# Performance work log

Measured on AMD Instinct MI355X. Metric: run time of the kernel, lower is better.

## Reference

```python
import jax, jax.numpy as jnp
import numpy as np

# Counts-based indexed grouped linear (canonical 'uv,u,v' path of
# SegmentedPolynomialIndexedLinear): tokens x[z] are sorted by group idx[z];
# output y[z] = coeff * x[z] @ W[idx[z]] where W = w.reshape(C, U, V).

C, U, V, Z = 8, 512, 512, 32768


def setup_inputs() -> dict:
    key = jax.random.key(0)
    kw, kx, ki = jax.random.split(key, 3)
    w = jax.random.normal(kw, (C, U * V), dtype=jnp.float32)  # [C, u*v] per-group weights
    x = jax.random.normal(kx, (Z, U), dtype=jnp.float32)      # [Z, u] tokens
    idx = jnp.sort(jax.random.randint(ki, (Z,), 0, C))        # sorted group ids (module asserts sortedness)
    coefficients = jnp.ones((1,), dtype=jnp.float32)          # path coefficient buffer
    return {"w": w, "x": x, "idx": idx, "coefficients": coefficients}


def reference(w, x, idx, coefficients):
    C_ = w.shape[0]
    Zt, U_ = x.shape
    V_ = w.shape[1] // U_
    Wg = w.reshape(C_, U_, V_)                                   # [C,u,v]
    # group membership (counts = bincount(idx) in the original; one-hot is its
    # dense, jit-friendly equivalent of the ragged grouped GEMM)
    onehot = (idx[:, None] == jnp.arange(C_)).astype(x.dtype)    # [Z,C]
    xg = jnp.einsum('zu,zc->czu', x, onehot)                     # [C,Z,u], zero outside own group
    y = jnp.einsum('czu,cuv->zv', xg, Wg)                        # [Z,v]
    return y * coefficients[0]
```

## Files before the change

kernel.cpp:

```cpp
#include <hip/hip_runtime.h>
#include <stdint.h>


#define Cg 8
#define Ud 512
#define Vd 512
#define Zd 32768

#define BM 128
#define BN 128
#define BK 32
#define KT 16

#define TILE_US 4096
#define NBN 4
#define NBM_MAX 263
#define GRID_GEMM (NBM_MAX * NBN)

#define WSW_US (Cg * NBN * KT * TILE_US)
#define WS_NEEDED ((size_t)WSW_US * 2 + 64)

typedef __attribute__((ext_vector_type(8))) short bf16x8;
typedef __attribute__((ext_vector_type(4))) float f32x4;
typedef __attribute__((ext_vector_type(4))) unsigned short us4;
typedef __attribute__((ext_vector_type(4))) float float4v;
typedef __attribute__((ext_vector_type(4))) unsigned int u32x4;

typedef __attribute__((address_space(3))) unsigned int lds_uint;
typedef const __attribute__((address_space(1))) unsigned int gbl_uint;

__device__ __forceinline__ unsigned short f2bf(float f) {
    unsigned int u = __float_as_uint(f);
    u += 0x7fffu + ((u >> 16) & 1u);
    return (unsigned short)(u >> 16);
}
__device__ __forceinline__ unsigned int pk2(float lo, float hi) {
    return (unsigned int)f2bf(lo) | ((unsigned int)f2bf(hi) << 16);
}



__global__ __launch_bounds__(256)
void convert_w(const float* __restrict__ w, const int* __restrict__ idx,
               unsigned short* __restrict__ wsw, int* __restrict__ starts)
{
    const int t = blockIdx.x * 256 + threadIdx.x;
    const int g   = t >> 16;
    const int rem = t & 65535;
    const int u0  = (rem >> 9) << 2;
    const int v   = rem & 511;
    const float* src = w + ((size_t)g << 18) + (size_t)u0 * Vd + v;
    us4 p;
    p[0] = f2bf(src[0]);
    p[1] = f2bf(src[Vd]);
    p[2] = f2bf(src[2 * Vd]);
    p[3] = f2bf(src[3 * Vd]);
    const int r = v & 127, k = u0 & 31;
    const int tile = (g * NBN + (v >> 7)) * KT + (u0 >> 5);
    const int off  = tile * TILE_US
                   + ((r >> 4) << 9) + ((k >> 3) << 7) + ((r & 15) << 3) + (k & 7);
    *(us4*)(wsw + off) = p;

    if (blockIdx.x == 0 && threadIdx.x < 9) {
        const int gq = threadIdx.x;
        int lo = 0;
        if (gq >= 8) lo = Zd;
        else {
            int hi = Zd;
            while (lo < hi) { int mid = (lo + hi) >> 1;
                              if (idx[mid] < gq) lo = mid + 1; else hi = mid; }
        }
        starts[gq] = lo;
    }
}


#define LDA(KTV, A0, A1, A2, A3) do {                                         \
    const float* p_ = ax + (KTV) * BK;                                        \
    A0 = *(const float4v*)(p_);                                               \
    A1 = *(const float4v*)(p_ + 4);                                           \
    A2 = *(const float4v*)(p_ + 8);                                           \
    A3 = *(const float4v*)(p_ + 12); } while (0)

#define CVW(BUF, A0, A1, A2, A3) do {                                         \
    u32x4 w1_, w2_;                                                           \
    w1_[0] = pk2(A0[0], A0[1]); w1_[1] = pk2(A0[2], A0[3]);                   \
    w1_[2] = pk2(A1[0], A1[1]); w1_[3] = pk2(A1[2], A1[3]);                   \
    w2_[0] = pk2(A2[0], A2[1]); w2_[1] = pk2(A2[2], A2[3]);                   \
    w2_[2] = pk2(A3[0], A3[1]); w2_[3] = pk2(A3[2], A3[3]);                   \
    *(u32x4*)(&BUF[aw])       = w1_;                                          \
    *(u32x4*)(&BUF[aw + 128]) = w2_; } while (0)

#define GLB(KTV, BUF) do {                                                    \
    const unsigned short* s_ = wB + (size_t)(KTV) * TILE_US;                  \
    __builtin_amdgcn_global_load_lds((gbl_uint*)(s_ + bo),                    \
                                     (lds_uint*)(&BUF[bo]), 16, 0, 0);        \
    __builtin_amdgcn_global_load_lds((gbl_uint*)(s_ + bo + 2048),             \
                                     (lds_uint*)(&BUF[bo + 2048]), 16, 0, 0); \
  } while (0)

#define CMP(ABUF, BBUF) do {                                                  \
    bf16x8 a_[4], b_[4];                                                      \
    _Pragma("unroll")                                                         \
    for (int mi_ = 0; mi_ < 4; ++mi_)                                         \
        a_[mi_] = *(const bf16x8*)(&ABUF[((wm4 + mi_) << 9) + fr]);           \
    _Pragma("unroll")                                                         \
    for (int ni_ = 0; ni_ < 4; ++ni_)                                         \
        b_[ni_] = *(const bf16x8*)(&BBUF[((wn4 + ni_) << 9) + fr]);           \
    _Pragma("unroll")                                                         \
    for (int mi_ = 0; mi_ < 4; ++mi_)                                         \
        _Pragma("unroll")                                                     \
        for (int ni_ = 0; ni_ < 4; ++ni_)                                     \
            acc[mi_][ni_] = __builtin_amdgcn_mfma_f32_16x16x32_bf16(          \
                a_[mi_], b_[ni_], acc[mi_][ni_], 0, 0, 0);                    \
  } while (0)

#define WAITBAR(N) do {                                                       \
    asm volatile("s_waitcnt vmcnt(" #N ") lgkmcnt(0)" ::: "memory");          \
    __builtin_amdgcn_s_barrier(); } while (0)

__global__ __launch_bounds__(256, 3)
void sgl_gemm(const float* __restrict__ x,
              const unsigned short* __restrict__ wsw,
              const int* __restrict__ starts,
              const float* __restrict__ coeff,
              float* __restrict__ y)
{
    __shared__ unsigned short As[2][TILE_US];
    __shared__ unsigned short Bs[2][TILE_US];

    const int tid = threadIdx.x, lane = tid & 63, wave = tid >> 6;
    const int l15 = lane & 15, l4 = lane >> 4;

    const int bid = blockIdx.x;
    const int xcd = bid & 7, io = bid >> 3;
    const int wk  = (xcd < 4) ? xcd * 132 + io : 528 + (xcd - 4) * 131 + io;
    const int bmp = wk >> 2, bn = wk & 3;

    int s[9];
#pragma unroll
    for (int i = 0; i < 9; ++i) s[i] = starts[i];
    int g = -1, lblk = 0, ab = 0;
#pragma unroll
    for (int gg = 0; gg < 8; ++gg) {
        const int c  = s[gg + 1] - s[gg];
        const int nb = (c + BM - 1) >> 7;
        if (g < 0 && bmp < ab + nb) { g = gg; lblk = bmp - ab; }
        ab += nb;
    }
    if (g < 0) return;
    const int start = s[g];
    const int cnt   = s[g + 1] - s[g];
    const int j0    = lblk << 7;

    const int ar = tid >> 1;
    const int ak = (tid & 1) << 4;
    const int rc = (j0 + ar < cnt) ? (j0 + ar) : (cnt - 1);
    const float* ax = x + (size_t)(start + rc) * Ud + ak;
    const int aw = ((ar >> 4) << 9) + ((ak >> 3) << 7) + ((ar & 15) << 3);

    const unsigned short* wB = wsw + (size_t)((g * NBN + bn) * KT) * TILE_US;
    const int bo = tid * 8;

    const int wm4 = (wave >> 1) << 2;
    const int wn4 = (wave & 1) << 2;
    const int fr  = (l4 << 7) + (l15 << 3);

    f32x4 acc[4][4];
#pragma unroll
    for (int mi = 0; mi < 4; ++mi)
#pragma unroll
        for (int ni = 0; ni < 4; ++ni)
            acc[mi][ni] = f32x4{0.f, 0.f, 0.f, 0.f};

    float4v e0, e1, e2, e3, o0, o1, o2, o3;

    LDA(0, e0, e1, e2, e3);
    __builtin_amdgcn_sched_barrier(0);
    GLB(0, Bs[0]);
    __builtin_amdgcn_sched_barrier(0);
    LDA(1, o0, o1, o2, o3);
    __builtin_amdgcn_sched_barrier(0);
    CVW(As[0], e0, e1, e2, e3);
    WAITBAR(4);

#pragma unroll
    for (int kt = 0; kt < 14; ++kt) {
        if ((kt & 1) == 0) {
            GLB(kt + 1, Bs[1]);
            __builtin_amdgcn_sched_barrier(0);
            LDA(kt + 2, e0, e1, e2, e3);
            __builtin_amdgcn_sched_barrier(0);
            CVW(As[1], o0, o1, o2, o3);
            CMP(As[0], Bs[0]);
        } else {
            GLB(kt + 1, Bs[0]);
            __builtin_amdgcn_sched_barrier(0);
            LDA(kt + 2, o0, o1, o2, o3);
            __builtin_amdgcn_sched_barrier(0);
            CVW(As[0], e0, e1, e2, e3);
            CMP(As[1], Bs[1]);
        }
        WAITBAR(4);
    }
    GLB(15, Bs[1]);
    __builtin_amdgcn_sched_barrier(0);
    CVW(As[1], o0, o1, o2, o3);
    CMP(As[0], Bs[0]);
    WAITBAR(0);
    CMP(As[1], Bs[1]);

    const float cf = coeff[0];
    const bool full = (j0 + BM) <= cnt;
#pragma unroll
    for (int mi = 0; mi < 4; ++mi) {
        const int rb = ((wave >> 1) << 6) + mi * 16 + l4 * 4;
#pragma unroll
        for (int ni = 0; ni < 4; ++ni) {
            const int c = bn * BN + ((wave & 1) << 6) + ni * 16 + l15;
#pragma unroll
            for (int q = 0; q < 4; ++q) {
                if (full || (j0 + rb + q) < cnt)
                    y[(size_t)(start + j0 + rb + q) * Vd + c] = acc[mi][ni][q] * cf;
            }
        }
    }
}


__global__ __launch_bounds__(256)
void sgl_naive(const float* __restrict__ w, const float* __restrict__ x,
               const int* __restrict__ idx, const float* __restrict__ coeff,
               float* __restrict__ y)
{
    __shared__ float xs[Ud];
    const int z = blockIdx.x;
    const int g = idx[z];
    for (int u = threadIdx.x; u < Ud; u += 256) xs[u] = x[(size_t)z * Ud + u];
    __syncthreads();
    const float* Wg = w + (size_t)g * (Ud * Vd);
    const float cf = coeff[0];
    for (int v = threadIdx.x; v < Vd; v += 256) {
        float acc = 0.f;
        for (int u = 0; u < Ud; ++u) acc += xs[u] * Wg[(size_t)u * Vd + v];
        y[(size_t)z * Vd + v] = acc * cf;
    }
}

extern "C" void kernel_launch(void* const* d_in, const int* in_sizes, int n_in,
                              void* d_out, int out_size, void* d_ws, size_t ws_size,
                              hipStream_t stream) {
    const float* w     = (const float*)d_in[0];
    const float* x     = (const float*)d_in[1];
    const int*   idx   = (const int*)d_in[2];
    const float* coeff = (const float*)d_in[3];
    float* y = (float*)d_out;

    if (ws_size >= WS_NEEDED) {
        unsigned short* wsw = (unsigned short*)d_ws;
        int* starts = (int*)((char*)d_ws + (size_t)WSW_US * 2);
        hipLaunchKernelGGL(convert_w, dim3(2048), dim3(256), 0, stream,
                           w, idx, wsw, starts);
        hipLaunchKernelGGL(sgl_gemm, dim3(GRID_GEMM), dim3(256), 0, stream,
                           x, wsw, starts, coeff, y);
    } else {
        hipLaunchKernelGGL(sgl_naive, dim3(Zd), dim3(256), 0, stream,
                           w, x, idx, coeff, y);
    }
}
```

Baseline: 51.18 us.

## Load A fragments directly to registers, skip LDS staging, triple-buffer B

Each lane now loads its x rows straight from global memory into registers in the MFMA fragment layout and converts to bf16 just before the MFMAs, so the A tile is no longer staged through LDS. B weights switch to a three-deep LDS ring with a single vmcnt wait and barrier per k-step. This removes the LDS writes and reads for A and one sync stage, but A loads become redundant across the two waves sharing rows, register pressure rises, and the occupancy hint drops from 3 to 2 blocks.

```diff
diff --git a/kernel.cpp b/kernel.cpp
--- a/kernel.cpp
+++ b/kernel.cpp
@@ -75,38 +75,36 @@
 }
 
 
-#define LDA(KTV, A0, A1, A2, A3) do {                                         \
-    const float* p_ = ax + (KTV) * BK;                                        \
-    A0 = *(const float4v*)(p_);                                               \
-    A1 = *(const float4v*)(p_ + 4);                                           \
-    A2 = *(const float4v*)(p_ + 8);                                           \
-    A3 = *(const float4v*)(p_ + 12); } while (0)
-
-#define CVW(BUF, A0, A1, A2, A3) do {                                         \
-    u32x4 w1_, w2_;                                                           \
-    w1_[0] = pk2(A0[0], A0[1]); w1_[1] = pk2(A0[2], A0[3]);                   \
-    w1_[2] = pk2(A1[0], A1[1]); w1_[3] = pk2(A1[2], A1[3]);                   \
-    w2_[0] = pk2(A2[0], A2[1]); w2_[1] = pk2(A2[2], A2[3]);                   \
-    w2_[2] = pk2(A3[0], A3[1]); w2_[3] = pk2(A3[2], A3[3]);                   \
-    *(u32x4*)(&BUF[aw])       = w1_;                                          \
-    *(u32x4*)(&BUF[aw + 128]) = w2_; } while (0)
-
-#define GLB(KTV, BUF) do {                                                    \
+#define LDA(KTV, BI) do {                                                     \
+    _Pragma("unroll")                                                         \
+    for (int mi_ = 0; mi_ < 4; ++mi_) {                                       \
+        const float* p_ = ap[mi_] + (KTV) * BK;                               \
+        ab[BI][mi_][0] = *(const float4v*)(p_);                               \
+        ab[BI][mi_][1] = *(const float4v*)(p_ + 4);                           \
+    } } while (0)
+
+#define GLB(KTV, J) do {                                                      \
     const unsigned short* s_ = wB + (size_t)(KTV) * TILE_US;                  \
     __builtin_amdgcn_global_load_lds((gbl_uint*)(s_ + bo),                    \
-                                     (lds_uint*)(&BUF[bo]), 16, 0, 0);        \
+                                     (lds_uint*)(&Bs[J][bo]), 16, 0, 0);      \
     __builtin_amdgcn_global_load_lds((gbl_uint*)(s_ + bo + 2048),             \
-                                     (lds_uint*)(&BUF[bo + 2048]), 16, 0, 0); \
+                                     (lds_uint*)(&Bs[J][bo + 2048]), 16, 0, 0); \
   } while (0)
 
-#define CMP(ABUF, BBUF) do {                                                  \
+#define CVT_CMP(BI, J) do {                                                   \
     bf16x8 a_[4], b_[4];                                                      \
     _Pragma("unroll")                                                         \
-    for (int mi_ = 0; mi_ < 4; ++mi_)                                         \
-        a_[mi_] = *(const bf16x8*)(&ABUF[((wm4 + mi_) << 9) + fr]);           \
+    for (int mi_ = 0; mi_ < 4; ++mi_) {                                       \
+        u32x4 t_;                                                             \
+        t_[0] = pk2(ab[BI][mi_][0][0], ab[BI][mi_][0][1]);                    \
+        t_[1] = pk2(ab[BI][mi_][0][2], ab[BI][mi_][0][3]);                    \
+        t_[2] = pk2(ab[BI][mi_][1][0], ab[BI][mi_][1][1]);                    \
+        t_[3] = pk2(ab[BI][mi_][1][2], ab[BI][mi_][1][3]);                    \
+        a_[mi_] = __builtin_bit_cast(bf16x8, t_);                             \
+    }                                                                         \
     _Pragma("unroll")                                                         \
     for (int ni_ = 0; ni_ < 4; ++ni_)                                         \
-        b_[ni_] = *(const bf16x8*)(&BBUF[((wn4 + ni_) << 9) + fr]);           \
+        b_[ni_] = *(const bf16x8*)(&Bs[J][((wn4 + ni_) << 9) + fr]);          \
     _Pragma("unroll")                                                         \
     for (int mi_ = 0; mi_ < 4; ++mi_)                                         \
         _Pragma("unroll")                                                     \
@@ -115,19 +113,16 @@
                 a_[mi_], b_[ni_], acc[mi_][ni_], 0, 0, 0);                    \
   } while (0)
 
-#define WAITBAR(N) do {                                                       \
-    asm volatile("s_waitcnt vmcnt(" #N ") lgkmcnt(0)" ::: "memory");          \
-    __builtin_amdgcn_s_barrier(); } while (0)
-
-__global__ __launch_bounds__(256, 3)
+#define WAITV(N) asm volatile("s_waitcnt vmcnt(" #N ")" ::: "memory")
+
+__global__ __launch_bounds__(256, 2)
 void sgl_gemm(const float* __restrict__ x,
               const unsigned short* __restrict__ wsw,
               const int* __restrict__ starts,
               const float* __restrict__ coeff,
               float* __restrict__ y)
 {
-    __shared__ unsigned short As[2][TILE_US];
-    __shared__ unsigned short Bs[2][TILE_US];
+    __shared__ unsigned short Bs[3][TILE_US];
 
     const int tid = threadIdx.x, lane = tid & 63, wave = tid >> 6;
     const int l15 = lane & 15, l4 = lane >> 4;
@@ -140,29 +135,30 @@
     int s[9];
 #pragma unroll
     for (int i = 0; i < 9; ++i) s[i] = starts[i];
-    int g = -1, lblk = 0, ab = 0;
+    int g = -1, lblk = 0, ab_ = 0;
 #pragma unroll
     for (int gg = 0; gg < 8; ++gg) {
         const int c  = s[gg + 1] - s[gg];
         const int nb = (c + BM - 1) >> 7;
-        if (g < 0 && bmp < ab + nb) { g = gg; lblk = bmp - ab; }
-        ab += nb;
+        if (g < 0 && bmp < ab_ + nb) { g = gg; lblk = bmp - ab_; }
+        ab_ += nb;
     }
     if (g < 0) return;
     const int start = s[g];
     const int cnt   = s[g + 1] - s[g];
     const int j0    = lblk << 7;
 
-    const int ar = tid >> 1;
-    const int ak = (tid & 1) << 4;
-    const int rc = (j0 + ar < cnt) ? (j0 + ar) : (cnt - 1);
-    const float* ax = x + (size_t)(start + rc) * Ud + ak;
-    const int aw = ((ar >> 4) << 9) + ((ak >> 3) << 7) + ((ar & 15) << 3);
+    const int wrow = (wave >> 1) * 64;
+    const float* ap[4];
+#pragma unroll
+    for (int mi = 0; mi < 4; ++mi) {
+        int r = j0 + wrow + mi * 16 + l15;
+        if (r >= cnt) r = cnt - 1;
+        ap[mi] = x + (size_t)(start + r) * Ud + (l4 << 3);
+    }
 
     const unsigned short* wB = wsw + (size_t)((g * NBN + bn) * KT) * TILE_US;
-    const int bo = tid * 8;
-
-    const int wm4 = (wave >> 1) << 2;
+    const int bo  = tid * 8;
     const int wn4 = (wave & 1) << 2;
     const int fr  = (l4 << 7) + (l15 << 3);
 
@@ -173,48 +169,32 @@
         for (int ni = 0; ni < 4; ++ni)
             acc[mi][ni] = f32x4{0.f, 0.f, 0.f, 0.f};
 
-    float4v e0, e1, e2, e3, o0, o1, o2, o3;
-
-    LDA(0, e0, e1, e2, e3);
+    float4v ab[2][4][2];
+
+    GLB(0, 0);
+    LDA(0, 0);
     __builtin_amdgcn_sched_barrier(0);
-    GLB(0, Bs[0]);
+    GLB(1, 1);
+
+#pragma unroll
+    for (int kt = 0; kt < 15; ++kt) {
+        LDA(kt + 1, (kt + 1) & 1);
+        WAITV(10);
+        __builtin_amdgcn_s_barrier();
+        __builtin_amdgcn_sched_barrier(0);
+        if (kt < 14) GLB(kt + 2, (kt + 2) % 3);
+        CVT_CMP(kt & 1, kt % 3);
+    }
+    WAITV(0);
+    __builtin_amdgcn_s_barrier();
     __builtin_amdgcn_sched_barrier(0);
-    LDA(1, o0, o1, o2, o3);
-    __builtin_amdgcn_sched_barrier(0);
-    CVW(As[0], e0, e1, e2, e3);
-    WAITBAR(4);
-
-#pragma unroll
-    for (int kt = 0; kt < 14; ++kt) {
-        if ((kt & 1) == 0) {
-            GLB(kt + 1, Bs[1]);
-            __builtin_amdgcn_sched_barrier(0);
-            LDA(kt + 2, e0, e1, e2, e3);
-            __builtin_amdgcn_sched_barrier(0);
-            CVW(As[1], o0, o1, o2, o3);
-            CMP(As[0], Bs[0]);
-        } else {
-            GLB(kt + 1, Bs[0]);
-            __builtin_amdgcn_sched_barrier(0);
-            LDA(kt + 2, o0, o1, o2, o3);
-            __builtin_amdgcn_sched_barrier(0);
-            CVW(As[0], e0, e1, e2, e3);
-            CMP(As[1], Bs[1]);
-        }
-        WAITBAR(4);
-    }
-    GLB(15, Bs[1]);
-    __builtin_amdgcn_sched_barrier(0);
-    CVW(As[1], o0, o1, o2, o3);
-    CMP(As[0], Bs[0]);
-    WAITBAR(0);
-    CMP(As[1], Bs[1]);
+    CVT_CMP(1, 0);
 
     const float cf = coeff[0];
     const bool full = (j0 + BM) <= cnt;
 #pragma unroll
     for (int mi = 0; mi < 4; ++mi) {
-        const int rb = ((wave >> 1) << 6) + mi * 16 + l4 * 4;
+        const int rb = wrow + mi * 16 + l4 * 4;
 #pragma unroll
         for (int ni = 0; ni < 4; ++ni) {
             const int c = bn * BN + ((wave & 1) << 6) + ni * 16 + l15;
```

Measured after the change: 95.53 us. +86.6%, slower.

## Remap A-tile loads for contiguous LDS writes, use hardware bf16 convert, raise occupancy

Applied to the files above, without the earlier changes.

Each thread now loads 8 floats from each of two rows (rA and rA+64) rather than 16 consecutive floats from one row. Its packed bf16 data then lands at tid*8 and tid*8+2048, so LDS stores are contiguous across the wavefront and avoid bank conflicts. The hand-written round-to-nearest bf16 conversion is replaced by the HIP __float2bfloat16 intrinsic, which may map to a native convert instruction. Launch bounds rise from 3 to 4 blocks per SM, which raises occupancy at the risk of register pressure or spills.

```diff
diff --git a/kernel.cpp b/kernel.cpp
--- a/kernel.cpp
+++ b/kernel.cpp
@@ -1,4 +1,5 @@
 #include <hip/hip_runtime.h>
+#include <hip/hip_bf16.h>
 #include <stdint.h>
 
 
@@ -29,13 +30,10 @@
 typedef __attribute__((address_space(3))) unsigned int lds_uint;
 typedef const __attribute__((address_space(1))) unsigned int gbl_uint;
 
-__device__ __forceinline__ unsigned short f2bf(float f) {
-    unsigned int u = __float_as_uint(f);
-    u += 0x7fffu + ((u >> 16) & 1u);
-    return (unsigned short)(u >> 16);
-}
 __device__ __forceinline__ unsigned int pk2(float lo, float hi) {
-    return (unsigned int)f2bf(lo) | ((unsigned int)f2bf(hi) << 16);
+    unsigned short l = __bfloat16_as_ushort(__float2bfloat16(lo));
+    unsigned short h = __bfloat16_as_ushort(__float2bfloat16(hi));
+    return (unsigned int)l | ((unsigned int)h << 16);
 }
 
 
@@ -51,10 +49,10 @@
     const int v   = rem & 511;
     const float* src = w + ((size_t)g << 18) + (size_t)u0 * Vd + v;
     us4 p;
-    p[0] = f2bf(src[0]);
-    p[1] = f2bf(src[Vd]);
-    p[2] = f2bf(src[2 * Vd]);
-    p[3] = f2bf(src[3 * Vd]);
+    p[0] = (unsigned short)__bfloat16_as_ushort(__float2bfloat16(src[0]));
+    p[1] = (unsigned short)__bfloat16_as_ushort(__float2bfloat16(src[Vd]));
+    p[2] = (unsigned short)__bfloat16_as_ushort(__float2bfloat16(src[2 * Vd]));
+    p[3] = (unsigned short)__bfloat16_as_ushort(__float2bfloat16(src[3 * Vd]));
     const int r = v & 127, k = u0 & 31;
     const int tile = (g * NBN + (v >> 7)) * KT + (u0 >> 5);
     const int off  = tile * TILE_US
@@ -76,11 +74,10 @@
 
 
 #define LDA(KTV, A0, A1, A2, A3) do {                                         \
-    const float* p_ = ax + (KTV) * BK;                                        \
-    A0 = *(const float4v*)(p_);                                               \
-    A1 = *(const float4v*)(p_ + 4);                                           \
-    A2 = *(const float4v*)(p_ + 8);                                           \
-    A3 = *(const float4v*)(p_ + 12); } while (0)
+    A0 = *(const float4v*)(ax0 + (KTV) * BK);                                 \
+    A1 = *(const float4v*)(ax0 + (KTV) * BK + 4);                             \
+    A2 = *(const float4v*)(ax1 + (KTV) * BK);                                 \
+    A3 = *(const float4v*)(ax1 + (KTV) * BK + 4); } while (0)
 
 #define CVW(BUF, A0, A1, A2, A3) do {                                         \
     u32x4 w1_, w2_;                                                           \
@@ -88,8 +85,8 @@
     w1_[2] = pk2(A1[0], A1[1]); w1_[3] = pk2(A1[2], A1[3]);                   \
     w2_[0] = pk2(A2[0], A2[1]); w2_[1] = pk2(A2[2], A2[3]);                   \
     w2_[2] = pk2(A3[0], A3[1]); w2_[3] = pk2(A3[2], A3[3]);                   \
-    *(u32x4*)(&BUF[aw])       = w1_;                                          \
-    *(u32x4*)(&BUF[aw + 128]) = w2_; } while (0)
+    *(u32x4*)(&BUF[aw])        = w1_;                                         \
+    *(u32x4*)(&BUF[aw + 2048]) = w2_; } while (0)
 
 #define GLB(KTV, BUF) do {                                                    \
     const unsigned short* s_ = wB + (size_t)(KTV) * TILE_US;                  \
@@ -119,7 +116,9 @@
     asm volatile("s_waitcnt vmcnt(" #N ") lgkmcnt(0)" ::: "memory");          \
     __builtin_amdgcn_s_barrier(); } while (0)
 
-__global__ __launch_bounds__(256, 3)
+#define SBAR() __builtin_amdgcn_sched_barrier(0)
+
+__global__ __launch_bounds__(256, 4)
 void sgl_gemm(const float* __restrict__ x,
               const unsigned short* __restrict__ wsw,
               const int* __restrict__ starts,
@@ -153,11 +152,13 @@
     const int cnt   = s[g + 1] - s[g];
     const int j0    = lblk << 7;
 
-    const int ar = tid >> 1;
-    const int ak = (tid & 1) << 4;
-    const int rc = (j0 + ar < cnt) ? (j0 + ar) : (cnt - 1);
-    const float* ax = x + (size_t)(start + rc) * Ud + ak;
-    const int aw = ((ar >> 4) << 9) + ((ak >> 3) << 7) + ((ar & 15) << 3);
+    const int rA = ((tid >> 6) << 4) + (tid & 15);
+    const int k0 = ((tid >> 4) & 3) << 3;
+    const int rc0 = (j0 + rA < cnt) ? (j0 + rA) : (cnt - 1);
+    const int rc1 = (j0 + rA + 64 < cnt) ? (j0 + rA + 64) : (cnt - 1);
+    const float* ax0 = x + (size_t)(start + rc0) * Ud + k0;
+    const float* ax1 = x + (size_t)(start + rc1) * Ud + k0;
+    const int aw = tid * 8;
 
     const unsigned short* wB = wsw + (size_t)((g * NBN + bn) * KT) * TILE_US;
     const int bo = tid * 8;
@@ -176,11 +177,11 @@
     float4v e0, e1, e2, e3, o0, o1, o2, o3;
 
     LDA(0, e0, e1, e2, e3);
-    __builtin_amdgcn_sched_barrier(0);
+    SBAR();
     GLB(0, Bs[0]);
-    __builtin_amdgcn_sched_barrier(0);
+    SBAR();
     LDA(1, o0, o1, o2, o3);
-    __builtin_amdgcn_sched_barrier(0);
+    SBAR();
     CVW(As[0], e0, e1, e2, e3);
     WAITBAR(4);
 
@@ -188,23 +189,23 @@
     for (int kt = 0; kt < 14; ++kt) {
         if ((kt & 1) == 0) {
             GLB(kt + 1, Bs[1]);
-            __builtin_amdgcn_sched_barrier(0);
+            SBAR();
             LDA(kt + 2, e0, e1, e2, e3);
-            __builtin_amdgcn_sched_barrier(0);
+            SBAR();
             CVW(As[1], o0, o1, o2, o3);
             CMP(As[0], Bs[0]);
         } else {
             GLB(kt + 1, Bs[0]);
-            __builtin_amdgcn_sched_barrier(0);
+            SBAR();
             LDA(kt + 2, o0, o1, o2, o3);
-            __builtin_amdgcn_sched_barrier(0);
+            SBAR();
             CVW(As[0], e0, e1, e2, e3);
             CMP(As[1], Bs[1]);
         }
         WAITBAR(4);
     }
     GLB(15, Bs[1]);
-    __builtin_amdgcn_sched_barrier(0);
+    SBAR();
     CVW(As[1], o0, o1, o2, o3);
     CMP(As[0], Bs[0]);
     WAITBAR(0);
```

New measurement: 63.47 us. 24.0% more time.
